# Kernel tuning notes

Measured on AMD Instinct MI355X. Metric: run time of the kernel, lower is better.

Reference implementation:

```python
import jax, jax.numpy as jnp
import numpy as np

L = 2048      # seq_len
E = 2048      # hidden_dim
H = 16        # num_heads
D = E // H    # head_dim


def setup_inputs() -> dict:
    key = jax.random.key(0)
    ks = jax.random.split(key, 6)
    x = jax.random.normal(ks[0], (L, E), dtype=jnp.float32)
    bias_matrix = jax.random.normal(ks[1], (L, L), dtype=jnp.float32) * 0.1
    # nn.MultiheadAttention params: packed in_proj [3E, E] + bias [3E], out_proj [E, E] + bias [E]
    in_proj_weight = jax.random.normal(ks[2], (3 * E, E), dtype=jnp.float32) * 0.02
    in_proj_bias = jax.random.normal(ks[3], (3 * E,), dtype=jnp.float32) * 0.02
    out_proj_weight = jax.random.normal(ks[4], (E, E), dtype=jnp.float32) * 0.02
    out_proj_bias = jax.random.normal(ks[5], (E,), dtype=jnp.float32) * 0.02
    return {
        "x": x,
        "bias_matrix": bias_matrix,
        "in_proj_weight": in_proj_weight,
        "in_proj_bias": in_proj_bias,
        "out_proj_weight": out_proj_weight,
        "out_proj_bias": out_proj_bias,
    }


def reference(x, bias_matrix, in_proj_weight, in_proj_bias, out_proj_weight, out_proj_bias):
    # Packed QKV projection (torch Linear convention: y = x @ W.T + b)
    qkv = x @ in_proj_weight.T + in_proj_bias            # [L, 3E]
    q, k, v = jnp.split(qkv, 3, axis=-1)                 # each [L, E]
    q = q.reshape(L, H, D)
    k = k.reshape(L, H, D)
    v = v.reshape(L, H, D)
    scale = 1.0 / jnp.sqrt(jnp.asarray(D, dtype=x.dtype))
    # scores: [H, L, L]; bias_matrix broadcast over heads (torch 2D attn_mask semantics)
    scores = jnp.einsum("lhd,mhd->hlm", q * scale, k) + bias_matrix[None, :, :]
    attn = jax.nn.softmax(scores, axis=-1)
    ctx = jnp.einsum("hlm,mhd->lhd", attn, v).reshape(L, E)
    out = ctx @ out_proj_weight.T + out_proj_bias        # [L, E]
    return out
```

## Files before the change

### kernel.cpp

```cpp
#include <hip/hip_runtime.h>
#include <math.h>

#define L_SEQ 2048
#define E_DIM 2048
#define H_NUM 16
#define D_HEAD 128

typedef __attribute__((ext_vector_type(8))) _Float16 half8;
typedef __attribute__((ext_vector_type(4))) _Float16 half4;
typedef __attribute__((ext_vector_type(4))) float floatx4;

static __device__ __forceinline__ void gload16(const void* g, void* lds) {
  __builtin_amdgcn_global_load_lds(
      (const __attribute__((address_space(1))) void*)g,
      (__attribute__((address_space(3))) void*)lds, 16, 0, 0);
}

__global__ __launch_bounds__(256)
void cvt3_f32_f16(const float* __restrict__ a, _Float16* __restrict__ oa, int na,
                  const float* __restrict__ b, _Float16* __restrict__ ob, int nb,
                  const float* __restrict__ c, _Float16* __restrict__ oc, int nc) {
  int i = (blockIdx.x * 256 + threadIdx.x) * 8;
  const float* src;
  _Float16* dst;
  if (i < na) {
    src = a + i; dst = oa + i;
  } else if (i < na + nb) {
    src = b + (i - na); dst = ob + (i - na);
  } else if (i < na + nb + nc) {
    src = c + (i - na - nb); dst = oc + (i - na - nb);
  } else {
    return;
  }
  float4 p = *(const float4*)src;
  float4 q = *(const float4*)(src + 4);
  half8 h = {(_Float16)p.x, (_Float16)p.y, (_Float16)p.z, (_Float16)p.w,
             (_Float16)q.x, (_Float16)q.y, (_Float16)q.z, (_Float16)q.w};
  *(half8*)dst = h;
}

__global__ __launch_bounds__(256)
void cvt_f32_f16(const float* __restrict__ in, _Float16* __restrict__ out, int n) {
  int i = (blockIdx.x * 256 + threadIdx.x) * 8;
  if (i >= n) return;
  float4 a = *(const float4*)(in + i);
  float4 b = *(const float4*)(in + i + 4);
  half8 h = {(_Float16)a.x, (_Float16)a.y, (_Float16)a.z, (_Float16)a.w,
             (_Float16)b.x, (_Float16)b.y, (_Float16)b.z, (_Float16)b.w};
  *(half8*)(out + i) = h;
}

template <int TM, int TN, int WR, int WC, int EPI>
__global__ __launch_bounds__(256)
void gemm_mfma(const _Float16* __restrict__ A, const _Float16* __restrict__ B,
               const float* __restrict__ bias, float* __restrict__ C,
               _Float16* __restrict__ qk, _Float16* __restrict__ vt,
               int M, int N, int K) {
  constexpr int RT = TM / (16 * WR);
  constexpr int CT = TN / (16 * WC);
  constexpr int ACH = TM / 8;
  constexpr int NCH = (TM + TN) / 32;

  __shared__ _Float16 As[TM * 64];
  __shared__ _Float16 Bs[TN * 64];

  const int tid = threadIdx.x;
  const int wave = tid >> 6, lane = tid & 63;
  const int l15 = lane & 15, quad = lane >> 4;
  const int wr = wave / WC, wc = wave % WC;
  const int row0 = blockIdx.y * TM, col0 = blockIdx.x * TN;

  const int srow = lane >> 3;
  const int gc = (lane & 7) ^ srow;

  floatx4 acc[RT][CT];
#pragma unroll
  for (int i = 0; i < RT; ++i)
#pragma unroll
    for (int j = 0; j < CT; ++j) acc[i][j] = (floatx4){0.f, 0.f, 0.f, 0.f};

  for (int k0 = 0; k0 < K; k0 += 64) {
    __syncthreads();
#pragma unroll
    for (int c = 0; c < NCH; ++c) {
      int chunk = wave * NCH + c;
      if (chunk < ACH) {
        int row = chunk * 8 + srow;
        gload16((const char*)(A + (size_t)(row0 + row) * K + k0) + gc * 16,
                (char*)As + chunk * 1024);
      } else {
        int bch = chunk - ACH;
        int row = bch * 8 + srow;
        gload16((const char*)(B + (size_t)(col0 + row) * K + k0) + gc * 16,
                (char*)Bs + bch * 1024);
      }
    }
    __syncthreads();

#pragma unroll
    for (int ks = 0; ks < 2; ++ks) {
      half8 af[RT], bf[CT];
#pragma unroll
      for (int t = 0; t < RT; ++t) {
        int r = wr * (16 * RT) + t * 16 + l15;
        af[t] = *(const half8*)&As[r * 64 + (((ks * 4 + quad) ^ (r & 7)) * 8)];
      }
#pragma unroll
      for (int t = 0; t < CT; ++t) {
        int r = wc * (16 * CT) + t * 16 + l15;
        bf[t] = *(const half8*)&Bs[r * 64 + (((ks * 4 + quad) ^ (r & 7)) * 8)];
      }
#pragma unroll
      for (int tr = 0; tr < RT; ++tr)
#pragma unroll
        for (int tc = 0; tc < CT; ++tc)
          acc[tr][tc] = __builtin_amdgcn_mfma_f32_16x16x32_f16(
              af[tr], bf[tc], acc[tr][tc], 0, 0, 0);
    }
  }

  const int crow = row0 + wr * (16 * RT);
  const int ccol = col0 + wc * (16 * CT);

  if (EPI == 0) {
#pragma unroll
    for (int tc = 0; tc < CT; ++tc) {
      int col = ccol + tc * 16 + l15;
      float bb = bias[col];
#pragma unroll
      for (int tr = 0; tr < RT; ++tr)
#pragma unroll
        for (int r = 0; r < 4; ++r)
          C[(size_t)(crow + tr * 16 + quad * 4 + r) * N + col] =
              acc[tr][tc][r] + bb;
    }
  } else if (col0 < 2 * E_DIM) {
#pragma unroll
    for (int tc = 0; tc < CT; ++tc) {
      int col = ccol + tc * 16 + l15;
      float bb = bias[col];
#pragma unroll
      for (int tr = 0; tr < RT; ++tr)
#pragma unroll
        for (int r = 0; r < 4; ++r)
          qk[(size_t)(crow + tr * 16 + quad * 4 + r) * (2 * E_DIM) + col] =
              (_Float16)(acc[tr][tc][r] + bb);
    }
  } else {
#pragma unroll
    for (int tc = 0; tc < CT; ++tc) {
      int col = ccol + tc * 16 + l15;
      float bb = bias[col];
      int vrow = col - 2 * E_DIM;
#pragma unroll
      for (int tr = 0; tr < RT; ++tr) {
        int rbase = crow + tr * 16 + quad * 4;
        half4 h = {(_Float16)(acc[tr][tc][0] + bb), (_Float16)(acc[tr][tc][1] + bb),
                   (_Float16)(acc[tr][tc][2] + bb), (_Float16)(acc[tr][tc][3] + bb)};
        *(half4*)&vt[(size_t)vrow * L_SEQ + rbase] = h;
      }
    }
  }
}

__global__ __launch_bounds__(256, 1)
void attn_mfma(const _Float16* __restrict__ qk, const _Float16* __restrict__ vt,
               const _Float16* __restrict__ bias16, _Float16* __restrict__ ctx) {
  const int h = blockIdx.x;
  const int q0 = blockIdx.y * 128;
  const int tid = threadIdx.x;
  const int wave = tid >> 6;
  const int lane = tid & 63;
  const int l15 = lane & 15;
  const int quad = lane >> 4;

  __shared__ _Float16 Ks[2][64][136];
  __shared__ _Float16 Vst[2][128][72];
  __shared__ _Float16 Ps[128][72];

  half8 qa[2][4];
#pragma unroll
  for (int rt = 0; rt < 2; ++rt) {
    const _Float16* qp = qk + (size_t)(q0 + wave * 32 + rt * 16 + l15) * (2 * E_DIM) +
                         h * D_HEAD + quad * 8;
#pragma unroll
    for (int ks = 0; ks < 4; ++ks) qa[rt][ks] = *(const half8*)(qp + ks * 32);
  }

  float l_i[2] = {0.f, 0.f};
  floatx4 o[2][8];
#pragma unroll
  for (int rt = 0; rt < 2; ++rt)
#pragma unroll
    for (int t = 0; t < 8; ++t) o[rt][t] = (floatx4){0.f, 0.f, 0.f, 0.f};

  const float scale = 0.088388347648318447f;

  half8 kreg[4], vreg[4];
  half4 bcur[2][4], bnxt[2][4];
#pragma unroll
  for (int c = 0; c < 4; ++c) {
    int m = c * 256 + tid;
    kreg[c] = *(const half8*)(qk + (size_t)(m >> 4) * (2 * E_DIM) + E_DIM +
                              h * D_HEAD + (m & 15) * 8);
    vreg[c] = *(const half8*)(vt + (size_t)(h * D_HEAD + (m >> 3)) * L_SEQ +
                              (m & 7) * 8);
  }
#pragma unroll
  for (int rt = 0; rt < 2; ++rt)
#pragma unroll
    for (int t = 0; t < 4; ++t)
      bcur[rt][t] = *(const half4*)&bias16[(size_t)(q0 + wave * 32 + rt * 16 + l15) *
                                               L_SEQ + 16 * t + quad * 4];
#pragma unroll
  for (int c = 0; c < 4; ++c) {
    int m = c * 256 + tid;
    *(half8*)&Ks[0][m >> 4][(m & 15) * 8] = kreg[c];
    *(half8*)&Vst[0][m >> 3][(m & 7) * 8] = vreg[c];
  }

#pragma unroll 2
  for (int it = 0; it < 32; ++it) {
    const int cur = it & 1, nxt = cur ^ 1;
    const int kt = it * 64;
    __syncthreads();

    if (it < 31) {
#pragma unroll
      for (int c = 0; c < 4; ++c) {
        int m = c * 256 + tid;
        kreg[c] = *(const half8*)(qk + (size_t)(kt + 64 + (m >> 4)) * (2 * E_DIM) +
                                  E_DIM + h * D_HEAD + (m & 15) * 8);
        vreg[c] = *(const half8*)(vt + (size_t)(h * D_HEAD + (m >> 3)) * L_SEQ +
                                  kt + 64 + (m & 7) * 8);
      }
#pragma unroll
      for (int rt = 0; rt < 2; ++rt)
#pragma unroll
        for (int t = 0; t < 4; ++t)
          bnxt[rt][t] =
              *(const half4*)&bias16[(size_t)(q0 + wave * 32 + rt * 16 + l15) *
                                         L_SEQ + kt + 64 + 16 * t + quad * 4];
    }

    floatx4 st[2][4];
#pragma unroll
    for (int t = 0; t < 4; ++t) {
      st[0][t] = (floatx4){0.f, 0.f, 0.f, 0.f};
      st[1][t] = (floatx4){0.f, 0.f, 0.f, 0.f};
    }
#pragma unroll
    for (int ks = 0; ks < 4; ++ks)
#pragma unroll
      for (int t = 0; t < 4; ++t) {
        half8 kf = *(const half8*)&Ks[cur][16 * t + l15][ks * 32 + quad * 8];
        st[0][t] = __builtin_amdgcn_mfma_f32_16x16x32_f16(kf, qa[0][ks], st[0][t], 0, 0, 0);
        st[1][t] = __builtin_amdgcn_mfma_f32_16x16x32_f16(kf, qa[1][ks], st[1][t], 0, 0, 0);
      }

#pragma unroll
    for (int rt = 0; rt < 2; ++rt) {
      float ls = 0.f;
      float ps[4][4];
#pragma unroll
      for (int t = 0; t < 4; ++t)
#pragma unroll
        for (int r = 0; r < 4; ++r) {
          float p = __expf(fmaf(st[rt][t][r], scale, (float)bcur[rt][t][r]));
          ps[t][r] = p;
          ls += p;
        }
      ls += __shfl_xor(ls, 16);
      ls += __shfl_xor(ls, 32);
      l_i[rt] += ls;
#pragma unroll
      for (int t = 0; t < 4; ++t) {
        half4 hp = {(_Float16)ps[t][0], (_Float16)ps[t][1],
                    (_Float16)ps[t][2], (_Float16)ps[t][3]};
        *(half4*)&Ps[wave * 32 + rt * 16 + l15][16 * t + quad * 4] = hp;
      }
    }

    half8 pa[2][2];
#pragma unroll
    for (int rt = 0; rt < 2; ++rt)
#pragma unroll
      for (int ks = 0; ks < 2; ++ks)
        pa[rt][ks] = *(const half8*)&Ps[wave * 32 + rt * 16 + l15][ks * 32 + quad * 8];
#pragma unroll
    for (int t = 0; t < 8; ++t) {
#pragma unroll
      for (int ks = 0; ks < 2; ++ks) {
        half8 vf = *(const half8*)&Vst[cur][16 * t + l15][ks * 32 + quad * 8];
        o[0][t] = __builtin_amdgcn_mfma_f32_16x16x32_f16(pa[0][ks], vf, o[0][t], 0, 0, 0);
        o[1][t] = __builtin_amdgcn_mfma_f32_16x16x32_f16(pa[1][ks], vf, o[1][t], 0, 0, 0);
      }
    }

    if (it < 31) {
#pragma unroll
      for (int c = 0; c < 4; ++c) {
        int m = c * 256 + tid;
        *(half8*)&Ks[nxt][m >> 4][(m & 15) * 8] = kreg[c];
        *(half8*)&Vst[nxt][m >> 3][(m & 7) * 8] = vreg[c];
      }
#pragma unroll
      for (int rt = 0; rt < 2; ++rt)
#pragma unroll
        for (int t = 0; t < 4; ++t) bcur[rt][t] = bnxt[rt][t];
    }
  }

#pragma unroll
  for (int rt = 0; rt < 2; ++rt) {
    float inv[4];
#pragma unroll
    for (int r = 0; r < 4; ++r) inv[r] = 1.f / __shfl(l_i[rt], quad * 4 + r);
#pragma unroll
    for (int t = 0; t < 8; ++t)
#pragma unroll
      for (int r = 0; r < 4; ++r) {
        int row = q0 + wave * 32 + rt * 16 + quad * 4 + r;
        ctx[(size_t)row * E_DIM + h * D_HEAD + 16 * t + l15] =
            (_Float16)(o[rt][t][r] * inv[r]);
      }
  }
}

extern "C" void kernel_launch(void* const* d_in, const int* in_sizes, int n_in,
                              void* d_out, int out_size, void* d_ws, size_t ws_size,
                              hipStream_t stream) {
  const float* x          = (const float*)d_in[0];
  const float* bias_mat   = (const float*)d_in[1];
  const float* in_proj_w  = (const float*)d_in[2];
  const float* in_proj_b  = (const float*)d_in[3];
  const float* out_proj_w = (const float*)d_in[4];
  const float* out_proj_b = (const float*)d_in[5];
  float* out = (float*)d_out;

  _Float16* x16 = (_Float16*)d_ws;
  _Float16* w1  = x16 + (size_t)L_SEQ * E_DIM;
  _Float16* w2  = w1 + (size_t)3 * E_DIM * E_DIM;
  _Float16* qk  = w2 + (size_t)E_DIM * E_DIM;
  _Float16* vt  = qk + (size_t)L_SEQ * 2 * E_DIM;
  _Float16* ctx = vt + (size_t)E_DIM * L_SEQ;
  _Float16* bias16 = x16;

  dim3 blk(256);
  const int nx = L_SEQ * E_DIM, nw1 = 3 * E_DIM * E_DIM, nw2 = E_DIM * E_DIM;

  cvt3_f32_f16<<<(nx + nw1 + nw2) / 2048, blk, 0, stream>>>(
      x, x16, nx, in_proj_w, w1, nw1, out_proj_w, w2, nw2);

  gemm_mfma<128, 128, 2, 2, 1><<<dim3(3 * E_DIM / 128, L_SEQ / 128), blk, 0, stream>>>(
      x16, w1, in_proj_b, nullptr, qk, vt, L_SEQ, 3 * E_DIM, E_DIM);

  cvt_f32_f16<<<(L_SEQ * L_SEQ) / 2048, blk, 0, stream>>>(bias_mat, bias16,
                                                          L_SEQ * L_SEQ);

  attn_mfma<<<dim3(H_NUM, L_SEQ / 128), blk, 0, stream>>>(qk, vt, bias16, ctx);

  gemm_mfma<128, 64, 4, 1, 0><<<dim3(E_DIM / 64, L_SEQ / 128), blk, 0, stream>>>(
      ctx, w2, out_proj_b, out, nullptr, nullptr, L_SEQ, E_DIM, E_DIM);
}
```

Before: 312.3 us.

## Double-buffer GEMM LDS tiles and read fp32 bias directly in attention

The GEMM kernel now uses two LDS buffers and issues the next K-tile's global-to-LDS loads before computing on the current one, so memory latency overlaps MFMA work. The separate kernel that converted the bias matrix to fp16 is removed, and the attention kernel loads the fp32 bias directly. This saves a launch and a conversion pass, but doubles the bias bytes each attention block reads (repeated across heads) and doubles GEMM LDS use.

After: 285.4 us. 1.09x faster.

```diff
diff --git a/kernel.cpp b/kernel.cpp
--- a/kernel.cpp
+++ b/kernel.cpp
@@ -39,17 +39,6 @@
   *(half8*)dst = h;
 }
 
-__global__ __launch_bounds__(256)
-void cvt_f32_f16(const float* __restrict__ in, _Float16* __restrict__ out, int n) {
-  int i = (blockIdx.x * 256 + threadIdx.x) * 8;
-  if (i >= n) return;
-  float4 a = *(const float4*)(in + i);
-  float4 b = *(const float4*)(in + i + 4);
-  half8 h = {(_Float16)a.x, (_Float16)a.y, (_Float16)a.z, (_Float16)a.w,
-             (_Float16)b.x, (_Float16)b.y, (_Float16)b.z, (_Float16)b.w};
-  *(half8*)(out + i) = h;
-}
-
 template <int TM, int TN, int WR, int WC, int EPI>
 __global__ __launch_bounds__(256)
 void gemm_mfma(const _Float16* __restrict__ A, const _Float16* __restrict__ B,
@@ -61,8 +50,8 @@
   constexpr int ACH = TM / 8;
   constexpr int NCH = (TM + TN) / 32;
 
-  __shared__ _Float16 As[TM * 64];
-  __shared__ _Float16 Bs[TN * 64];
+  __shared__ _Float16 As[2][TM * 64];
+  __shared__ _Float16 Bs[2][TN * 64];
 
   const int tid = threadIdx.x;
   const int wave = tid >> 6, lane = tid & 63;
@@ -73,29 +62,36 @@
   const int srow = lane >> 3;
   const int gc = (lane & 7) ^ srow;
 
-  floatx4 acc[RT][CT];
-#pragma unroll
-  for (int i = 0; i < RT; ++i)
-#pragma unroll
-    for (int j = 0; j < CT; ++j) acc[i][j] = (floatx4){0.f, 0.f, 0.f, 0.f};
-
-  for (int k0 = 0; k0 < K; k0 += 64) {
-    __syncthreads();
+  auto stage = [&](int buf, int k0) {
 #pragma unroll
     for (int c = 0; c < NCH; ++c) {
       int chunk = wave * NCH + c;
       if (chunk < ACH) {
         int row = chunk * 8 + srow;
         gload16((const char*)(A + (size_t)(row0 + row) * K + k0) + gc * 16,
-                (char*)As + chunk * 1024);
+                (char*)&As[buf][0] + chunk * 1024);
       } else {
         int bch = chunk - ACH;
         int row = bch * 8 + srow;
         gload16((const char*)(B + (size_t)(col0 + row) * K + k0) + gc * 16,
-                (char*)Bs + bch * 1024);
-      }
-    }
+                (char*)&Bs[buf][0] + bch * 1024);
+      }
+    }
+  };
+
+  floatx4 acc[RT][CT];
+#pragma unroll
+  for (int i = 0; i < RT; ++i)
+#pragma unroll
+    for (int j = 0; j < CT; ++j) acc[i][j] = (floatx4){0.f, 0.f, 0.f, 0.f};
+
+  const int niter = K / 64;
+  stage(0, 0);
+
+  for (int it = 0; it < niter; ++it) {
+    const int cur = it & 1;
     __syncthreads();
+    if (it + 1 < niter) stage(cur ^ 1, (it + 1) * 64);
 
 #pragma unroll
     for (int ks = 0; ks < 2; ++ks) {
@@ -103,12 +99,12 @@
 #pragma unroll
       for (int t = 0; t < RT; ++t) {
         int r = wr * (16 * RT) + t * 16 + l15;
-        af[t] = *(const half8*)&As[r * 64 + (((ks * 4 + quad) ^ (r & 7)) * 8)];
+        af[t] = *(const half8*)&As[cur][r * 64 + (((ks * 4 + quad) ^ (r & 7)) * 8)];
       }
 #pragma unroll
       for (int t = 0; t < CT; ++t) {
         int r = wc * (16 * CT) + t * 16 + l15;
-        bf[t] = *(const half8*)&Bs[r * 64 + (((ks * 4 + quad) ^ (r & 7)) * 8)];
+        bf[t] = *(const half8*)&Bs[cur][r * 64 + (((ks * 4 + quad) ^ (r & 7)) * 8)];
       }
 #pragma unroll
       for (int tr = 0; tr < RT; ++tr)
@@ -165,7 +161,7 @@
 
 __global__ __launch_bounds__(256, 1)
 void attn_mfma(const _Float16* __restrict__ qk, const _Float16* __restrict__ vt,
-               const _Float16* __restrict__ bias16, _Float16* __restrict__ ctx) {
+               const float* __restrict__ bias, _Float16* __restrict__ ctx) {
   const int h = blockIdx.x;
   const int q0 = blockIdx.y * 128;
   const int tid = threadIdx.x;
@@ -197,7 +193,7 @@
   const float scale = 0.088388347648318447f;
 
   half8 kreg[4], vreg[4];
-  half4 bcur[2][4], bnxt[2][4];
+  floatx4 bcur[2][4], bnxt[2][4];
 #pragma unroll
   for (int c = 0; c < 4; ++c) {
     int m = c * 256 + tid;
@@ -210,7 +206,7 @@
   for (int rt = 0; rt < 2; ++rt)
 #pragma unroll
     for (int t = 0; t < 4; ++t)
-      bcur[rt][t] = *(const half4*)&bias16[(size_t)(q0 + wave * 32 + rt * 16 + l15) *
+      bcur[rt][t] = *(const floatx4*)&bias[(size_t)(q0 + wave * 32 + rt * 16 + l15) *
                                                L_SEQ + 16 * t + quad * 4];
 #pragma unroll
   for (int c = 0; c < 4; ++c) {
@@ -239,7 +235,7 @@
 #pragma unroll
         for (int t = 0; t < 4; ++t)
           bnxt[rt][t] =
-              *(const half4*)&bias16[(size_t)(q0 + wave * 32 + rt * 16 + l15) *
+              *(const floatx4*)&bias[(size_t)(q0 + wave * 32 + rt * 16 + l15) *
                                          L_SEQ + kt + 64 + 16 * t + quad * 4];
     }
 
@@ -266,7 +262,7 @@
       for (int t = 0; t < 4; ++t)
 #pragma unroll
         for (int r = 0; r < 4; ++r) {
-          float p = __expf(fmaf(st[rt][t][r], scale, (float)bcur[rt][t][r]));
+          float p = __expf(fmaf(st[rt][t][r], scale, bcur[rt][t][r]));
           ps[t][r] = p;
           ls += p;
         }
@@ -344,7 +340,6 @@
   _Float16* qk  = w2 + (size_t)E_DIM * E_DIM;
   _Float16* vt  = qk + (size_t)L_SEQ * 2 * E_DIM;
   _Float16* ctx = vt + (size_t)E_DIM * L_SEQ;
-  _Float16* bias16 = x16;
 
   dim3 blk(256);
   const int nx = L_SEQ * E_DIM, nw1 = 3 * E_DIM * E_DIM, nw2 = E_DIM * E_DIM;
@@ -355,10 +350,7 @@
   gemm_mfma<128, 128, 2, 2, 1><<<dim3(3 * E_DIM / 128, L_SEQ / 128), blk, 0, stream>>>(
       x16, w1, in_proj_b, nullptr, qk, vt, L_SEQ, 3 * E_DIM, E_DIM);
 
-  cvt_f32_f16<<<(L_SEQ * L_SEQ) / 2048, blk, 0, stream>>>(bias_mat, bias16,
-                                                          L_SEQ * L_SEQ);
-
-  attn_mfma<<<dim3(H_NUM, L_SEQ / 128), blk, 0, stream>>>(qk, vt, bias16, ctx);
+  attn_mfma<<<dim3(H_NUM, L_SEQ / 128), blk, 0, stream>>>(qk, vt, bias_mat, ctx);
 
   gemm_mfma<128, 64, 4, 1, 0><<<dim3(E_DIM / 64, L_SEQ / 128), blk, 0, stream>>>(
       ctx, w2, out_proj_b, out, nullptr, nullptr, L_SEQ, E_DIM, E_DIM);
```
